# Performance work log

Hardware: AMD Instinct MI355X
Metric: run time of the kernel (lower is better)

The kernel has to match this reference:

```python
import jax, jax.numpy as jnp
import numpy as np

GROUP_SIZE = 128
SCALE_MIN = 1e-8
IN_FEATURES = 4096
OUT_FEATURES = 4096
BATCH, SEQ = 4, 2048


def quantize_literati(weight, scales):
    """w -> sign(w) * clamp(scale) per group of GROUP_SIZE along last dim.
    in_features is divisible by GROUP_SIZE, so no padding branch is needed.
    """
    O, C = weight.shape
    wg = weight.reshape(O, C // GROUP_SIZE, GROUP_SIZE)
    # torch.sign with zeros mapped to +1
    signs = jnp.where(wg >= 0, 1.0, -1.0).astype(weight.dtype)
    s = jnp.maximum(scales, SCALE_MIN)  # (O, num_groups)
    w_q = signs * s[..., None]
    return w_q.reshape(O, C)


def setup_inputs() -> dict:
    key = jax.random.key(0)
    kx, kw = jax.random.split(key)
    x = jax.random.normal(kx, (BATCH, SEQ, IN_FEATURES), dtype=jnp.float32)
    # kaiming_uniform_(a=sqrt(5)) -> U(-1/sqrt(fan_in), 1/sqrt(fan_in))
    bound = 1.0 / np.sqrt(IN_FEATURES)
    weight = jax.random.uniform(kw, (OUT_FEATURES, IN_FEATURES), dtype=jnp.float32,
                                minval=-bound, maxval=bound)
    scales = jnp.full((OUT_FEATURES, IN_FEATURES // GROUP_SIZE), 0.1, dtype=jnp.float32)
    return {"x": x, "weight": weight, "scales": scales}


def reference(x, weight, scales):
    w_q = quantize_literati(weight, scales)
    # F.linear: x @ w_q.T
    return jnp.einsum('bsc,oc->bso', x, w_q)
```

## Files before the change

### kernel.cpp

```cpp
#include <hip/hip_runtime.h>
#include <hip/hip_bf16.h>
#include <stdint.h>
#include <stddef.h>


#define M_DIM 8192
#define N_DIM 4096
#define K_DIM 4096
#define BM 256
#define BN 256
#define BK 32
#define NT (K_DIM / BK)

typedef __bf16 bf16x8 __attribute__((ext_vector_type(8)));
typedef float f32x4 __attribute__((ext_vector_type(4)));

__device__ __forceinline__ void async_copy16(const void* g, void* l) {
  __builtin_amdgcn_global_load_lds((__attribute__((address_space(1))) void*)g,
                                   (__attribute__((address_space(3))) void*)l,
                                   16, 0, 0);
}

#define X_THREADS ((size_t)M_DIM * K_DIM / 16)
#define W_THREADS ((size_t)N_DIM * K_DIM / 16)
__global__ __launch_bounds__(256) void prep_kernel(
    const float* __restrict__ x, const float* __restrict__ w,
    const float* __restrict__ scales, __bf16* __restrict__ xb,
    __bf16* __restrict__ wb) {
  const size_t t = (size_t)blockIdx.x * blockDim.x + threadIdx.x;
  if (t < X_THREADS) {
    const float4* src = (const float4*)x + t * 4;
    bf16x8* dst = (bf16x8*)xb + t * 2;
#pragma unroll
    for (int h = 0; h < 2; ++h) {
      const float4 v0 = src[h * 2 + 0];
      const float4 v1 = src[h * 2 + 1];
      bf16x8 o;
      o[0] = (__bf16)v0.x; o[1] = (__bf16)v0.y;
      o[2] = (__bf16)v0.z; o[3] = (__bf16)v0.w;
      o[4] = (__bf16)v1.x; o[5] = (__bf16)v1.y;
      o[6] = (__bf16)v1.z; o[7] = (__bf16)v1.w;
      dst[h] = o;
    }
  } else {
    const size_t u = t - X_THREADS;
    const size_t idx = u * 16;
    const int o_ = (int)(idx >> 12);
    const int grp = (int)(idx & 4095) >> 7;
    const float s = fmaxf(scales[(o_ << 5) + grp], 1e-8f);
    const float4* src = (const float4*)w + u * 4;
    bf16x8* dst = (bf16x8*)wb + u * 2;
#pragma unroll
    for (int h = 0; h < 2; ++h) {
      const float4 v0 = src[h * 2 + 0];
      const float4 v1 = src[h * 2 + 1];
      bf16x8 q;
      q[0] = (__bf16)((v0.x >= 0.f) ? s : -s);
      q[1] = (__bf16)((v0.y >= 0.f) ? s : -s);
      q[2] = (__bf16)((v0.z >= 0.f) ? s : -s);
      q[3] = (__bf16)((v0.w >= 0.f) ? s : -s);
      q[4] = (__bf16)((v1.x >= 0.f) ? s : -s);
      q[5] = (__bf16)((v1.y >= 0.f) ? s : -s);
      q[6] = (__bf16)((v1.z >= 0.f) ? s : -s);
      q[7] = (__bf16)((v1.w >= 0.f) ? s : -s);
      dst[h] = q;
    }
  }
}


#define LDS_A(b) ((char*)lds + (b) * 32768)
#define LDS_B(b) ((char*)lds + (b) * 32768 + 16384)

#define STAGE_A_TO(b) do {                        \
    char* _d = LDS_A(b);                          \
    async_copy16(aP0, _d + dO0);                  \
    async_copy16(aP1, _d + dO1);                  \
  } while (0)

#define STAGE_B_TO(b) do {                        \
    char* _d = LDS_B(b);                          \
    async_copy16(bP0, _d + dO0);                  \
    async_copy16(bP1, _d + dO1);                  \
  } while (0)

#define ADVANCE do { aP0 += BK; aP1 += BK; bP0 += BK; bP1 += BK; } while (0)

#define TILE_BODY(BUF, DO_STAGE, VMSTR) do {                                   \
    char* _bufA = LDS_A(BUF);                                                  \
    char* _bufB = LDS_B(BUF);                                                  \
    bf16x8 _av0[4], _av1[4], _bv[4];                                           \
       \
    _Pragma("unroll") for (int _i = 0; _i < 4; ++_i)                           \
      _av0[_i] = *(const bf16x8*)(_bufA + aOff[0][_i]);                        \
    _Pragma("unroll") for (int _j = 0; _j < 4; ++_j)                           \
      _bv[_j] = *(const bf16x8*)(_bufB + bOff[_j]);                            \
    _Pragma("unroll") for (int _i = 0; _i < 4; ++_i)                           \
      _av1[_i] = *(const bf16x8*)(_bufA + aOff[1][_i]);                        \
    if (DO_STAGE) STAGE_A_TO((BUF + 3) & 3);                                   \
    __builtin_amdgcn_s_barrier();                                              \
    __builtin_amdgcn_s_setprio(1);                                             \
    _Pragma("unroll") for (int _i = 0; _i < 4; ++_i)                           \
      _Pragma("unroll") for (int _j = 0; _j < 4; ++_j)                         \
        acc[_i][_j] = __builtin_amdgcn_mfma_f32_16x16x32_bf16(                 \
            _av0[_i], _bv[_j], acc[_i][_j], 0, 0, 0);                          \
    __builtin_amdgcn_s_setprio(0);                                             \
    __builtin_amdgcn_s_barrier();                                              \
    if (DO_STAGE) { STAGE_B_TO((BUF + 3) & 3); ADVANCE; }                      \
    __builtin_amdgcn_s_barrier();                                              \
    __builtin_amdgcn_s_setprio(1);                                             \
    _Pragma("unroll") for (int _i = 0; _i < 4; ++_i)                           \
      _Pragma("unroll") for (int _j = 0; _j < 4; ++_j)                         \
        acc[4 + _i][_j] = __builtin_amdgcn_mfma_f32_16x16x32_bf16(             \
            _av1[_i], _bv[_j], acc[4 + _i][_j], 0, 0, 0);                      \
    __builtin_amdgcn_s_setprio(0);                                             \
    asm volatile("s_waitcnt " VMSTR ::: "memory");                             \
    __builtin_amdgcn_s_barrier();                                              \
    __builtin_amdgcn_sched_barrier(0);    \
  } while (0)

__global__ __launch_bounds__(512, 2) void literati_gemm(
    const __bf16* __restrict__ Ab, const __bf16* __restrict__ Bb,
    float* __restrict__ C) {
  __shared__ __align__(16) char lds[4 * 32768];

  const int tid = threadIdx.x;
  const int lane = tid & 63;
  const int wave = tid >> 6;
  const int bn0 = blockIdx.x * BN;
  const int bm0 = blockIdx.y * BM;
  const int wm = wave >> 2;
  const int wn = wave & 3;

  const int r_in = lane >> 2;
  const int kc_st = (lane & 3) ^ ((lane >> 3) & 3);
  const int c0 = wave * 2;
  const __bf16* aP0 = Ab + (size_t)(bm0 + c0 * 16 + r_in) * K_DIM + kc_st * 8;
  const __bf16* aP1 = Ab + (size_t)(bm0 + (c0 + 1) * 16 + r_in) * K_DIM + kc_st * 8;
  const __bf16* bP0 = Bb + (size_t)(bn0 + c0 * 16 + r_in) * K_DIM + kc_st * 8;
  const __bf16* bP1 = Bb + (size_t)(bn0 + (c0 + 1) * 16 + r_in) * K_DIM + kc_st * 8;
  const int dO0 = (c0 * 64 + lane) * 16;
  const int dO1 = ((c0 + 1) * 64 + lane) * 16;

  const int fr = lane & 15;
  const int kc_rd = lane >> 4;
  int aOff[2][4], bOff[4];
#pragma unroll
  for (int mh = 0; mh < 2; ++mh)
#pragma unroll
    for (int i = 0; i < 4; ++i) {
      const int row = wm * 128 + mh * 64 + i * 16 + fr;
      aOff[mh][i] = (row * 4 + (kc_rd ^ ((row >> 1) & 3))) * 16;
    }
#pragma unroll
  for (int j = 0; j < 4; ++j) {
    const int row = wn * 64 + j * 16 + fr;
    bOff[j] = (row * 4 + (kc_rd ^ ((row >> 1) & 3))) * 16;
  }

  f32x4 acc[8][4];
#pragma unroll
  for (int f = 0; f < 8; ++f)
#pragma unroll
    for (int j = 0; j < 4; ++j)
#pragma unroll
      for (int r = 0; r < 4; ++r) acc[f][j][r] = 0.f;

  STAGE_A_TO(0); STAGE_B_TO(0); ADVANCE;
  STAGE_A_TO(1); STAGE_B_TO(1); ADVANCE;
  STAGE_A_TO(2); STAGE_B_TO(2); ADVANCE;
  asm volatile("s_waitcnt vmcnt(8)" ::: "memory");
  __builtin_amdgcn_s_barrier();
  __builtin_amdgcn_sched_barrier(0);

  for (int tq = 0; tq < 31; ++tq) {
    TILE_BODY(0, 1, "vmcnt(8)");
    TILE_BODY(1, 1, "vmcnt(8)");
    TILE_BODY(2, 1, "vmcnt(8)");
    TILE_BODY(3, 1, "vmcnt(8)");
  }
  TILE_BODY(0, 1, "vmcnt(8)");
  TILE_BODY(1, 0, "vmcnt(4)");
  TILE_BODY(2, 0, "vmcnt(0)");
  TILE_BODY(3, 0, "vmcnt(0)");

  const int col0 = bn0 + wn * 64 + fr;
  const int rbase = bm0 + wm * 128 + (lane >> 4) * 4;
#pragma unroll
  for (int mh = 0; mh < 2; ++mh)
#pragma unroll
    for (int i = 0; i < 4; ++i) {
      const int row0 = rbase + mh * 64 + i * 16;
#pragma unroll
      for (int j = 0; j < 4; ++j) {
        float* p = C + (size_t)row0 * N_DIM + col0 + j * 16;
#pragma unroll
        for (int r = 0; r < 4; ++r)
          p[(size_t)r * N_DIM] = acc[mh * 4 + i][j][r];
      }
    }
}

extern "C" void kernel_launch(void* const* d_in, const int* in_sizes, int n_in,
                              void* d_out, int out_size, void* d_ws, size_t ws_size,
                              hipStream_t stream) {
  (void)in_sizes; (void)n_in; (void)out_size; (void)ws_size;
  const float* x = (const float*)d_in[0];
  const float* w = (const float*)d_in[1];
  const float* sc = (const float*)d_in[2];
  float* out = (float*)d_out;

  __bf16* xb = (__bf16*)d_ws;
  __bf16* wb = xb + (size_t)M_DIM * K_DIM;

  const size_t total_threads = X_THREADS + W_THREADS;
  prep_kernel<<<(int)(total_threads / 256), 256, 0, stream>>>(x, w, sc, xb, wb);

  dim3 grid(N_DIM / BN, M_DIM / BM);
  literati_gemm<<<grid, 512, 0, stream>>>(xb, wb, out);
}
```

Measured before the change: 486.2 us.

## Use 4 waves with 128x128 per-wave tiles instead of 8 waves

The GEMM block drops from 512 to 256 threads. Each wave now computes a 128x128 output sub-tile (8x8 MFMA fragments) instead of 128x64, raising register-level reuse of LDS fragments. Each thread issues four async copies per operand per stage, and the tile body is simplified to one MFMA phase with fewer barriers. The 8x8 f32x4 accumulators need 256 accumulator registers per thread, which raises register pressure and risks spilling. With half the waves there is also less latency hiding.

```diff
diff --git a/kernel.cpp b/kernel.cpp
--- a/kernel.cpp
+++ b/kernel.cpp
@@ -74,52 +74,53 @@
 
 #define STAGE_A_TO(b) do {                        \
     char* _d = LDS_A(b);                          \
-    async_copy16(aP0, _d + dO0);                  \
-    async_copy16(aP1, _d + dO1);                  \
+    async_copy16(aP0, _d + dA0);                  \
+    async_copy16(aP1, _d + dA1);                  \
+    async_copy16(aP2, _d + dA2);                  \
+    async_copy16(aP3, _d + dA3);                  \
   } while (0)
 
 #define STAGE_B_TO(b) do {                        \
     char* _d = LDS_B(b);                          \
-    async_copy16(bP0, _d + dO0);                  \
-    async_copy16(bP1, _d + dO1);                  \
-  } while (0)
-
-#define ADVANCE do { aP0 += BK; aP1 += BK; bP0 += BK; bP1 += BK; } while (0)
+    async_copy16(bP0, _d + dA0);                  \
+    async_copy16(bP1, _d + dA1);                  \
+    async_copy16(bP2, _d + dA2);                  \
+    async_copy16(bP3, _d + dA3);                  \
+  } while (0)
+
+#define ADVANCE do {                              \
+    aP0 += BK; aP1 += BK; aP2 += BK; aP3 += BK;   \
+    bP0 += BK; bP1 += BK; bP2 += BK; bP3 += BK;   \
+  } while (0)
 
 #define TILE_BODY(BUF, DO_STAGE, VMSTR) do {                                   \
     char* _bufA = LDS_A(BUF);                                                  \
     char* _bufB = LDS_B(BUF);                                                  \
-    bf16x8 _av0[4], _av1[4], _bv[4];                                           \
-       \
-    _Pragma("unroll") for (int _i = 0; _i < 4; ++_i)                           \
-      _av0[_i] = *(const bf16x8*)(_bufA + aOff[0][_i]);                        \
-    _Pragma("unroll") for (int _j = 0; _j < 4; ++_j)                           \
+    bf16x8 _av[8], _bv[8];                                                     \
+    _av[0] = *(const bf16x8*)(_bufA + aOff[0]);                                \
+    _av[1] = *(const bf16x8*)(_bufA + aOff[1]);                                \
+    _bv[0] = *(const bf16x8*)(_bufB + bOff[0]);                                \
+    _bv[1] = *(const bf16x8*)(_bufB + bOff[1]);                                \
+    if (DO_STAGE) { STAGE_A_TO((BUF + 3) & 3); STAGE_B_TO((BUF + 3) & 3); }    \
+    _Pragma("unroll") for (int _j = 2; _j < 8; ++_j)                           \
       _bv[_j] = *(const bf16x8*)(_bufB + bOff[_j]);                            \
-    _Pragma("unroll") for (int _i = 0; _i < 4; ++_i)                           \
-      _av1[_i] = *(const bf16x8*)(_bufA + aOff[1][_i]);                        \
-    if (DO_STAGE) STAGE_A_TO((BUF + 3) & 3);                                   \
-    __builtin_amdgcn_s_barrier();                                              \
-    __builtin_amdgcn_s_setprio(1);                                             \
-    _Pragma("unroll") for (int _i = 0; _i < 4; ++_i)                           \
-      _Pragma("unroll") for (int _j = 0; _j < 4; ++_j)                         \
-        acc[_i][_j] = __builtin_amdgcn_mfma_f32_16x16x32_bf16(                 \
-            _av0[_i], _bv[_j], acc[_i][_j], 0, 0, 0);                          \
-    __builtin_amdgcn_s_setprio(0);                                             \
-    __builtin_amdgcn_s_barrier();                                              \
-    if (DO_STAGE) { STAGE_B_TO((BUF + 3) & 3); ADVANCE; }                      \
-    __builtin_amdgcn_s_barrier();                                              \
-    __builtin_amdgcn_s_setprio(1);                                             \
-    _Pragma("unroll") for (int _i = 0; _i < 4; ++_i)                           \
-      _Pragma("unroll") for (int _j = 0; _j < 4; ++_j)                         \
-        acc[4 + _i][_j] = __builtin_amdgcn_mfma_f32_16x16x32_bf16(             \
-            _av1[_i], _bv[_j], acc[4 + _i][_j], 0, 0, 0);                      \
-    __builtin_amdgcn_s_setprio(0);                                             \
+    _Pragma("unroll") for (int _i = 2; _i < 8; ++_i)                           \
+      _av[_i] = *(const bf16x8*)(_bufA + aOff[_i]);                            \
+    if (DO_STAGE) ADVANCE;                                                     \
+    _Pragma("unroll") for (int _ip = 0; _ip < 4; ++_ip)                        \
+      _Pragma("unroll") for (int _jp = 0; _jp < 4; ++_jp)                      \
+        _Pragma("unroll") for (int _di = 0; _di < 2; ++_di)                    \
+          _Pragma("unroll") for (int _dj = 0; _dj < 2; ++_dj)                  \
+            acc[_ip * 2 + _di][_jp * 2 + _dj] =                                \
+                __builtin_amdgcn_mfma_f32_16x16x32_bf16(                       \
+                    _av[_ip * 2 + _di], _bv[_jp * 2 + _dj],                    \
+                    acc[_ip * 2 + _di][_jp * 2 + _dj], 0, 0, 0);               \
     asm volatile("s_waitcnt " VMSTR ::: "memory");                             \
     __builtin_amdgcn_s_barrier();                                              \
     __builtin_amdgcn_sched_barrier(0);    \
   } while (0)
 
-__global__ __launch_bounds__(512, 2) void literati_gemm(
+__global__ __launch_bounds__(256, 1) void literati_gemm(
     const __bf16* __restrict__ Ab, const __bf16* __restrict__ Bb,
     float* __restrict__ C) {
   __shared__ __align__(16) char lds[4 * 32768];
@@ -129,76 +130,75 @@
   const int wave = tid >> 6;
   const int bn0 = blockIdx.x * BN;
   const int bm0 = blockIdx.y * BM;
-  const int wm = wave >> 2;
-  const int wn = wave & 3;
+  const int wm = wave >> 1;
+  const int wn = wave & 1;
 
   const int r_in = lane >> 2;
   const int kc_st = (lane & 3) ^ ((lane >> 3) & 3);
-  const int c0 = wave * 2;
-  const __bf16* aP0 = Ab + (size_t)(bm0 + c0 * 16 + r_in) * K_DIM + kc_st * 8;
-  const __bf16* aP1 = Ab + (size_t)(bm0 + (c0 + 1) * 16 + r_in) * K_DIM + kc_st * 8;
-  const __bf16* bP0 = Bb + (size_t)(bn0 + c0 * 16 + r_in) * K_DIM + kc_st * 8;
-  const __bf16* bP1 = Bb + (size_t)(bn0 + (c0 + 1) * 16 + r_in) * K_DIM + kc_st * 8;
-  const int dO0 = (c0 * 64 + lane) * 16;
-  const int dO1 = ((c0 + 1) * 64 + lane) * 16;
+  const int s0 = wave * 4;
+  const __bf16* aP0 = Ab + (size_t)(bm0 + (s0 + 0) * 16 + r_in) * K_DIM + kc_st * 8;
+  const __bf16* aP1 = Ab + (size_t)(bm0 + (s0 + 1) * 16 + r_in) * K_DIM + kc_st * 8;
+  const __bf16* aP2 = Ab + (size_t)(bm0 + (s0 + 2) * 16 + r_in) * K_DIM + kc_st * 8;
+  const __bf16* aP3 = Ab + (size_t)(bm0 + (s0 + 3) * 16 + r_in) * K_DIM + kc_st * 8;
+  const __bf16* bP0 = Bb + (size_t)(bn0 + (s0 + 0) * 16 + r_in) * K_DIM + kc_st * 8;
+  const __bf16* bP1 = Bb + (size_t)(bn0 + (s0 + 1) * 16 + r_in) * K_DIM + kc_st * 8;
+  const __bf16* bP2 = Bb + (size_t)(bn0 + (s0 + 2) * 16 + r_in) * K_DIM + kc_st * 8;
+  const __bf16* bP3 = Bb + (size_t)(bn0 + (s0 + 3) * 16 + r_in) * K_DIM + kc_st * 8;
+  const int dA0 = ((s0 + 0) * 64 + lane) * 16;
+  const int dA1 = ((s0 + 1) * 64 + lane) * 16;
+  const int dA2 = ((s0 + 2) * 64 + lane) * 16;
+  const int dA3 = ((s0 + 3) * 64 + lane) * 16;
 
   const int fr = lane & 15;
   const int kc_rd = lane >> 4;
-  int aOff[2][4], bOff[4];
-#pragma unroll
-  for (int mh = 0; mh < 2; ++mh)
-#pragma unroll
-    for (int i = 0; i < 4; ++i) {
-      const int row = wm * 128 + mh * 64 + i * 16 + fr;
-      aOff[mh][i] = (row * 4 + (kc_rd ^ ((row >> 1) & 3))) * 16;
-    }
-#pragma unroll
-  for (int j = 0; j < 4; ++j) {
-    const int row = wn * 64 + j * 16 + fr;
-    bOff[j] = (row * 4 + (kc_rd ^ ((row >> 1) & 3))) * 16;
-  }
-
-  f32x4 acc[8][4];
-#pragma unroll
-  for (int f = 0; f < 8; ++f)
-#pragma unroll
-    for (int j = 0; j < 4; ++j)
-#pragma unroll
-      for (int r = 0; r < 4; ++r) acc[f][j][r] = 0.f;
+  int aOff[8], bOff[8];
+#pragma unroll
+  for (int i = 0; i < 8; ++i) {
+    const int rowa = wm * 128 + i * 16 + fr;
+    aOff[i] = (rowa * 4 + (kc_rd ^ ((rowa >> 1) & 3))) * 16;
+    const int rowb = wn * 128 + i * 16 + fr;
+    bOff[i] = (rowb * 4 + (kc_rd ^ ((rowb >> 1) & 3))) * 16;
+  }
+
+  f32x4 acc[8][8];
+#pragma unroll
+  for (int i = 0; i < 8; ++i)
+#pragma unroll
+    for (int j = 0; j < 8; ++j)
+#pragma unroll
+      for (int r = 0; r < 4; ++r) acc[i][j][r] = 0.f;
 
   STAGE_A_TO(0); STAGE_B_TO(0); ADVANCE;
   STAGE_A_TO(1); STAGE_B_TO(1); ADVANCE;
   STAGE_A_TO(2); STAGE_B_TO(2); ADVANCE;
-  asm volatile("s_waitcnt vmcnt(8)" ::: "memory");
+  asm volatile("s_waitcnt vmcnt(16)" ::: "memory");
   __builtin_amdgcn_s_barrier();
   __builtin_amdgcn_sched_barrier(0);
 
   for (int tq = 0; tq < 31; ++tq) {
-    TILE_BODY(0, 1, "vmcnt(8)");
-    TILE_BODY(1, 1, "vmcnt(8)");
-    TILE_BODY(2, 1, "vmcnt(8)");
-    TILE_BODY(3, 1, "vmcnt(8)");
-  }
-  TILE_BODY(0, 1, "vmcnt(8)");
-  TILE_BODY(1, 0, "vmcnt(4)");
+    TILE_BODY(0, 1, "vmcnt(16)");
+    TILE_BODY(1, 1, "vmcnt(16)");
+    TILE_BODY(2, 1, "vmcnt(16)");
+    TILE_BODY(3, 1, "vmcnt(16)");
+  }
+  TILE_BODY(0, 1, "vmcnt(16)");
+  TILE_BODY(1, 0, "vmcnt(8)");
   TILE_BODY(2, 0, "vmcnt(0)");
   TILE_BODY(3, 0, "vmcnt(0)");
 
-  const int col0 = bn0 + wn * 64 + fr;
-  const int rbase = bm0 + wm * 128 + (lane >> 4) * 4;
-#pragma unroll
-  for (int mh = 0; mh < 2; ++mh)
-#pragma unroll
-    for (int i = 0; i < 4; ++i) {
-      const int row0 = rbase + mh * 64 + i * 16;
-#pragma unroll
-      for (int j = 0; j < 4; ++j) {
-        float* p = C + (size_t)row0 * N_DIM + col0 + j * 16;
-#pragma unroll
-        for (int r = 0; r < 4; ++r)
-          p[(size_t)r * N_DIM] = acc[mh * 4 + i][j][r];
-      }
+  const int col0 = bn0 + wn * 128 + fr;
+  const int rb = bm0 + wm * 128 + (lane >> 4) * 4;
+#pragma unroll
+  for (int i = 0; i < 8; ++i) {
+    const int row0 = rb + i * 16;
+#pragma unroll
+    for (int j = 0; j < 8; ++j) {
+      float* p = C + (size_t)row0 * N_DIM + col0 + j * 16;
+#pragma unroll
+      for (int r = 0; r < 4; ++r)
+        p[(size_t)r * N_DIM] = acc[i][j][r];
     }
+  }
 }
 
 extern "C" void kernel_launch(void* const* d_in, const int* in_sizes, int n_in,
@@ -217,5 +217,5 @@
   prep_kernel<<<(int)(total_threads / 256), 256, 0, stream>>>(x, w, sc, xb, wb);
 
   dim3 grid(N_DIM / BN, M_DIM / BM);
-  literati_gemm<<<grid, 512, 0, stream>>>(xb, wb, out);
-}
+  literati_gemm<<<grid, 256, 0, stream>>>(xb, wb, out);
+}
```

Result: slower. 539.4 us (+10.9%).

## Switch GEMM to 32x32x16 MFMA with cross-tile LDS fragment prefetch

Applied to the files above, without the earlier changes.

Replaces the 16x16x32 bf16 MFMA tiling with 32x32x16 MFMAs (4x2 accumulators of 16 floats per wave), cutting LDS fragment reads per tile. The LDS reads for the first k-half of the next buffer are issued before the second MFMA batch, and two intra-tile barriers plus one staged load per wait are removed, so the vmcnt thresholds drop. It trades fewer instructions and barriers for longer MFMA latency and possible LDS read/write races from the removed barriers. The epilogue is rewritten for the 32x32 output layout.

```diff
diff --git a/kernel.cpp b/kernel.cpp
--- a/kernel.cpp
+++ b/kernel.cpp
@@ -13,7 +13,7 @@
 #define NT (K_DIM / BK)
 
 typedef __bf16 bf16x8 __attribute__((ext_vector_type(8)));
-typedef float f32x4 __attribute__((ext_vector_type(4)));
+typedef float f32x16 __attribute__((ext_vector_type(16)));
 
 __device__ __forceinline__ void async_copy16(const void* g, void* l) {
   __builtin_amdgcn_global_load_lds((__attribute__((address_space(1))) void*)g,
@@ -86,37 +86,40 @@
 
 #define ADVANCE do { aP0 += BK; aP1 += BK; bP0 += BK; bP1 += BK; } while (0)
 
-#define TILE_BODY(BUF, DO_STAGE, VMSTR) do {                                   \
-    char* _bufA = LDS_A(BUF);                                                  \
-    char* _bufB = LDS_B(BUF);                                                  \
-    bf16x8 _av0[4], _av1[4], _bv[4];                                           \
-       \
+#define TILE_BODY(BUF, DO_STAGE, DO_READN, VMSTR) do {                         \
+    char* _bA = LDS_A(BUF);                                                    \
+    char* _bB = LDS_B(BUF);                                                    \
+    char* _nA = LDS_A((BUF + 1) & 3);                                          \
+    char* _nB = LDS_B((BUF + 1) & 3);                                          \
+                 \
     _Pragma("unroll") for (int _i = 0; _i < 4; ++_i)                           \
-      _av0[_i] = *(const bf16x8*)(_bufA + aOff[0][_i]);                        \
-    _Pragma("unroll") for (int _j = 0; _j < 4; ++_j)                           \
-      _bv[_j] = *(const bf16x8*)(_bufB + bOff[_j]);                            \
-    _Pragma("unroll") for (int _i = 0; _i < 4; ++_i)                           \
-      _av1[_i] = *(const bf16x8*)(_bufA + aOff[1][_i]);                        \
+      F1a[_i] = *(const bf16x8*)(_bA + aOff[_i][1]);                           \
+    _Pragma("unroll") for (int _j = 0; _j < 2; ++_j)                           \
+      F1b[_j] = *(const bf16x8*)(_bB + bOff[_j][1]);                           \
     if (DO_STAGE) STAGE_A_TO((BUF + 3) & 3);                                   \
-    __builtin_amdgcn_s_barrier();                                              \
     __builtin_amdgcn_s_setprio(1);                                             \
     _Pragma("unroll") for (int _i = 0; _i < 4; ++_i)                           \
-      _Pragma("unroll") for (int _j = 0; _j < 4; ++_j)                         \
-        acc[_i][_j] = __builtin_amdgcn_mfma_f32_16x16x32_bf16(                 \
-            _av0[_i], _bv[_j], acc[_i][_j], 0, 0, 0);                          \
+      _Pragma("unroll") for (int _j = 0; _j < 2; ++_j)                         \
+        acc[_i][_j] = __builtin_amdgcn_mfma_f32_32x32x16_bf16(                 \
+            F0a[_i], F0b[_j], acc[_i][_j], 0, 0, 0);                           \
     __builtin_amdgcn_s_setprio(0);                                             \
-    __builtin_amdgcn_s_barrier();                                              \
+                 \
+    if (DO_READN) {                                                            \
+      _Pragma("unroll") for (int _i = 0; _i < 4; ++_i)                         \
+        F0a[_i] = *(const bf16x8*)(_nA + aOff[_i][0]);                         \
+      _Pragma("unroll") for (int _j = 0; _j < 2; ++_j)                         \
+        F0b[_j] = *(const bf16x8*)(_nB + bOff[_j][0]);                         \
+    }                                                                          \
     if (DO_STAGE) { STAGE_B_TO((BUF + 3) & 3); ADVANCE; }                      \
-    __builtin_amdgcn_s_barrier();                                              \
     __builtin_amdgcn_s_setprio(1);                                             \
     _Pragma("unroll") for (int _i = 0; _i < 4; ++_i)                           \
-      _Pragma("unroll") for (int _j = 0; _j < 4; ++_j)                         \
-        acc[4 + _i][_j] = __builtin_amdgcn_mfma_f32_16x16x32_bf16(             \
-            _av1[_i], _bv[_j], acc[4 + _i][_j], 0, 0, 0);                      \
+      _Pragma("unroll") for (int _j = 0; _j < 2; ++_j)                         \
+        acc[_i][_j] = __builtin_amdgcn_mfma_f32_32x32x16_bf16(                 \
+            F1a[_i], F1b[_j], acc[_i][_j], 0, 0, 0);                           \
     __builtin_amdgcn_s_setprio(0);                                             \
     asm volatile("s_waitcnt " VMSTR ::: "memory");                             \
     __builtin_amdgcn_s_barrier();                                              \
-    __builtin_amdgcn_sched_barrier(0);    \
+    __builtin_amdgcn_sched_barrier(0);                \
   } while (0)
 
 __global__ __launch_bounds__(512, 2) void literati_gemm(
@@ -142,63 +145,75 @@
   const int dO0 = (c0 * 64 + lane) * 16;
   const int dO1 = ((c0 + 1) * 64 + lane) * 16;
 
-  const int fr = lane & 15;
-  const int kc_rd = lane >> 4;
-  int aOff[2][4], bOff[4];
-#pragma unroll
-  for (int mh = 0; mh < 2; ++mh)
-#pragma unroll
-    for (int i = 0; i < 4; ++i) {
-      const int row = wm * 128 + mh * 64 + i * 16 + fr;
-      aOff[mh][i] = (row * 4 + (kc_rd ^ ((row >> 1) & 3))) * 16;
-    }
-#pragma unroll
-  for (int j = 0; j < 4; ++j) {
-    const int row = wn * 64 + j * 16 + fr;
-    bOff[j] = (row * 4 + (kc_rd ^ ((row >> 1) & 3))) * 16;
-  }
-
-  f32x4 acc[8][4];
-#pragma unroll
-  for (int f = 0; f < 8; ++f)
-#pragma unroll
-    for (int j = 0; j < 4; ++j)
-#pragma unroll
-      for (int r = 0; r < 4; ++r) acc[f][j][r] = 0.f;
+  const int m32 = lane & 31;
+  const int hl = lane >> 5;
+  int aOff[4][2], bOff[2][2];
+#pragma unroll
+  for (int i = 0; i < 4; ++i) {
+    const int row = wm * 128 + i * 32 + m32;
+#pragma unroll
+    for (int ks = 0; ks < 2; ++ks) {
+      const int kc = 2 * ks + hl;
+      aOff[i][ks] = (row * 4 + (kc ^ ((row >> 1) & 3))) * 16;
+    }
+  }
+#pragma unroll
+  for (int j = 0; j < 2; ++j) {
+    const int row = wn * 64 + j * 32 + m32;
+#pragma unroll
+    for (int ks = 0; ks < 2; ++ks) {
+      const int kc = 2 * ks + hl;
+      bOff[j][ks] = (row * 4 + (kc ^ ((row >> 1) & 3))) * 16;
+    }
+  }
+
+  f32x16 acc[4][2];
+#pragma unroll
+  for (int i = 0; i < 4; ++i)
+#pragma unroll
+    for (int j = 0; j < 2; ++j)
+#pragma unroll
+      for (int r = 0; r < 16; ++r) acc[i][j][r] = 0.f;
+
+  bf16x8 F0a[4], F0b[2], F1a[4], F1b[2];
 
   STAGE_A_TO(0); STAGE_B_TO(0); ADVANCE;
   STAGE_A_TO(1); STAGE_B_TO(1); ADVANCE;
   STAGE_A_TO(2); STAGE_B_TO(2); ADVANCE;
-  asm volatile("s_waitcnt vmcnt(8)" ::: "memory");
+  asm volatile("s_waitcnt vmcnt(4)" ::: "memory");
   __builtin_amdgcn_s_barrier();
   __builtin_amdgcn_sched_barrier(0);
+#pragma unroll
+  for (int i = 0; i < 4; ++i)
+    F0a[i] = *(const bf16x8*)(LDS_A(0) + aOff[i][0]);
+#pragma unroll
+  for (int j = 0; j < 2; ++j)
+    F0b[j] = *(const bf16x8*)(LDS_B(0) + bOff[j][0]);
 
   for (int tq = 0; tq < 31; ++tq) {
-    TILE_BODY(0, 1, "vmcnt(8)");
-    TILE_BODY(1, 1, "vmcnt(8)");
-    TILE_BODY(2, 1, "vmcnt(8)");
-    TILE_BODY(3, 1, "vmcnt(8)");
-  }
-  TILE_BODY(0, 1, "vmcnt(8)");
-  TILE_BODY(1, 0, "vmcnt(4)");
-  TILE_BODY(2, 0, "vmcnt(0)");
-  TILE_BODY(3, 0, "vmcnt(0)");
-
-  const int col0 = bn0 + wn * 64 + fr;
-  const int rbase = bm0 + wm * 128 + (lane >> 4) * 4;
-#pragma unroll
-  for (int mh = 0; mh < 2; ++mh)
-#pragma unroll
-    for (int i = 0; i < 4; ++i) {
-      const int row0 = rbase + mh * 64 + i * 16;
-#pragma unroll
-      for (int j = 0; j < 4; ++j) {
-        float* p = C + (size_t)row0 * N_DIM + col0 + j * 16;
-#pragma unroll
-        for (int r = 0; r < 4; ++r)
-          p[(size_t)r * N_DIM] = acc[mh * 4 + i][j][r];
+    TILE_BODY(0, 1, 1, "vmcnt(4)");
+    TILE_BODY(1, 1, 1, "vmcnt(4)");
+    TILE_BODY(2, 1, 1, "vmcnt(4)");
+    TILE_BODY(3, 1, 1, "vmcnt(4)");
+  }
+  TILE_BODY(0, 1, 1, "vmcnt(4)");
+  TILE_BODY(1, 0, 1, "vmcnt(0)");
+  TILE_BODY(2, 0, 1, "vmcnt(0)");
+  TILE_BODY(3, 0, 0, "vmcnt(0)");
+
+#pragma unroll
+  for (int i = 0; i < 4; ++i) {
+#pragma unroll
+    for (int j = 0; j < 2; ++j) {
+      const int col = bn0 + wn * 64 + j * 32 + m32;
+      const int rbase = bm0 + wm * 128 + i * 32 + 4 * hl;
+#pragma unroll
+      for (int r = 0; r < 16; ++r) {
+        const int row = rbase + (r & 3) + 8 * (r >> 2);
+        C[(size_t)row * N_DIM + col] = acc[i][j][r];
       }
     }
+  }
 }
 
 extern "C" void kernel_launch(void* const* d_in, const int* in_sizes, int n_in,
```

Result: no change. 481.5 us (-1.0%).
